# Kernel tuning notes

Hardware: AMD Instinct MI355X
Metric: run time of the kernel (lower is better)

Reference implementation:

```python
import jax, jax.numpy as jnp
import numpy as np

N, C, P, K = 100000, 64, 64, 16  # points, in_planes, planes, nsample
EPS = 1e-5

def _bn(y, g, b, m, v):
    # inference-mode batchnorm over channel (last) dim
    return (y - m) * (g * jax.lax.rsqrt(v + EPS)) + b

def setup_inputs() -> dict:
    key = jax.random.key(0)
    ks = jax.random.split(key, 12)
    p = jax.random.normal(ks[0], (N, 3), jnp.float32)
    x = jax.random.normal(ks[1], (N, C), jnp.float32)
    idx = jax.random.randint(ks[2], (N, K), 0, N, jnp.int32)
    s = 0.05
    w1 = jax.random.normal(ks[3], (C, P), jnp.float32) * s
    conv_w = jax.random.normal(ks[4], (P, P + 3), jnp.float32) * s  # Conv1d(P+3, P, 1) weight squeezed
    w3 = jax.random.normal(ks[5], (P, P), jnp.float32) * s
    def bn_params(k):
        k1, k2 = jax.random.split(k)
        return (jnp.ones((P,), jnp.float32),                      # gamma
                jnp.zeros((P,), jnp.float32),                     # beta
                jax.random.normal(k1, (P,), jnp.float32) * 0.01,  # running mean
                jnp.abs(jax.random.normal(k2, (P,), jnp.float32)) * 0.1 + 1.0)  # running var
    g1, b1, m1, v1 = bn_params(ks[6])
    g2, b2, m2, v2 = bn_params(ks[7])
    g3, b3, m3, v3 = bn_params(ks[8])
    return dict(p=p, x=x, idx=idx, w1=w1, g1=g1, b1=b1, m1=m1, v1=v1,
                conv_w=conv_w, g2=g2, b2=b2, m2=m2, v2=v2,
                w3=w3, g3=g3, b3=b3, m3=m3, v3=v3)

def reference(p, x, idx, w1, g1, b1, m1, v1, conv_w, g2, b2, m2, v2, w3, g3, b3, m3, v3):
    identity = x
    h = jax.nn.relu(_bn(x @ w1, g1, b1, m1, v1))                     # [N, P]
    # queryandgroup with use_xyz=True: concat(relative xyz, neighbor feats)
    rel = p[idx] - p[:, None, :]                                      # [N, K, 3]
    grouped = jnp.concatenate([rel, h[idx]], axis=-1)                 # [N, K, 3+P]
    e = jnp.einsum('nkc,oc->nko', grouped, conv_w)                    # conv1x1 -> [N, K, P]
    e = jax.nn.relu(_bn(e, g2, b2, m2, v2))
    f = jnp.max(e, axis=1)                                            # max over neighbors -> [N, P]
    out = jax.nn.relu(_bn(f @ w3, g3, b3, m3, v3) + identity)         # [N, P]
    return out
```

## Files before the change

### kernel.cpp

```cpp
#include <hip/hip_runtime.h>
#include <stdint.h>


#define EPS 1e-5f

typedef unsigned short u16;
typedef unsigned int u32;
typedef __attribute__((ext_vector_type(8))) short bf16x8;
typedef __attribute__((ext_vector_type(4))) float f32x4;

__device__ __forceinline__ float b2f(u16 u) { return __uint_as_float(((u32)u) << 16); }
__device__ __forceinline__ u16 f2b(float f) {
    u32 u = __float_as_uint(f);
    u32 r = u + 0x7fffu + ((u >> 16) & 1u);
    return (u16)(r >> 16);
}
__device__ __forceinline__ bool is_bf16(const void* g) { return ((const u32*)g)[0] == 0x3F803F80u; }
__device__ __forceinline__ float ldval(const void* p, size_t i, bool isbf) {
    return isbf ? b2f(((const u16*)p)[i]) : ((const float*)p)[i];
}
#define MFMA16(a, b, c) __builtin_amdgcn_mfma_f32_16x16x32_bf16(a, b, c, 0, 0, 0)

__device__ __forceinline__ bf16x8 asbf(uint4 u) {
    union { uint4 u; bf16x8 b; } c;
    c.u = u;
    return c.b;
}

__device__ __forceinline__ bf16x8 ldrow8(const void* base, size_t row, int coff, bool isbf) {
    if (isbf) {
        const u16* pp = (const u16*)base + row * 64 + coff;
        return asbf(*(const uint4*)pp);
    } else {
        const float* pp = (const float*)base + row * 64 + coff;
        float4 q0 = ((const float4*)pp)[0], q1 = ((const float4*)pp)[1];
        bf16x8 r;
        r[0] = (short)f2b(q0.x); r[1] = (short)f2b(q0.y);
        r[2] = (short)f2b(q0.z); r[3] = (short)f2b(q0.w);
        r[4] = (short)f2b(q1.x); r[5] = (short)f2b(q1.y);
        r[6] = (short)f2b(q1.z); r[7] = (short)f2b(q1.w);
        return r;
    }
}

__global__ void __launch_bounds__(256)
k_prep(const void* __restrict__ w1, const void* __restrict__ cw, const void* __restrict__ w3,
       const void* __restrict__ g1, const void* __restrict__ b1, const void* __restrict__ m1,
       const void* __restrict__ v1, const void* __restrict__ g2, const void* __restrict__ b2,
       const void* __restrict__ m2, const void* __restrict__ v2, const void* __restrict__ g3,
       const void* __restrict__ b3, const void* __restrict__ m3, const void* __restrict__ v3,
       uint4* __restrict__ w1f, uint4* __restrict__ cwf, uint4* __restrict__ w3f,
       float* __restrict__ bnst) {
    const bool isbf = is_bf16(g1);
    const int tid = blockIdx.x * blockDim.x + threadIdx.x;
    if (tid < 512) {
        int f = tid >> 6, lane = tid & 63;
        int ch = f >> 2, t = f & 3, quad = lane >> 4, c0 = lane & 15;
        union { uint4 u; bf16x8 b; } r;
#pragma unroll
        for (int j = 0; j < 8; ++j) {
            int c = ch * 32 + quad * 8 + j, o = t * 16 + c0;
            r.b[j] = (short)f2b(ldval(w1, (size_t)c * 64 + o, isbf));
        }
        w1f[f * 64 + lane] = r.u;
    } else if (tid < 1280) {
        int f = (tid - 512) >> 6, lane = tid & 63;
        int ch = f >> 2, t = f & 3, quad = lane >> 4, c0 = lane & 15;
        union { uint4 u; bf16x8 b; } r;
#pragma unroll
        for (int j = 0; j < 8; ++j) {
            int o = t * 16 + c0;
            short val;
            if (ch < 2) {
                int c = ch * 32 + quad * 8 + j;
                val = (short)f2b(ldval(cw, (size_t)o * 67 + 3 + c, isbf));
            } else {
                int pc = quad * 8 + j;
                val = (pc < 3) ? (short)f2b(ldval(cw, (size_t)o * 67 + pc, isbf)) : (short)0;
            }
            r.b[j] = val;
        }
        cwf[f * 64 + lane] = r.u;
    } else if (tid < 1792) {
        int f = (tid - 1280) >> 6, lane = tid & 63;
        int ch = f >> 2, t = f & 3, quad = lane >> 4, c0 = lane & 15;
        union { uint4 u; bf16x8 b; } r;
#pragma unroll
        for (int j = 0; j < 8; ++j) {
            int c = ch * 32 + quad * 8 + j, o = t * 16 + c0;
            r.b[j] = (short)f2b(ldval(w3, (size_t)c * 64 + o, isbf));
        }
        w3f[f * 64 + lane] = r.u;
    } else if (tid < 2176) {
        int id = tid - 1792;
        int bn = id >> 7, rem = id & 127, ch = rem & 63, which = rem >> 6;
        const void* g = (bn == 0) ? g1 : (bn == 1) ? g2 : g3;
        const void* b = (bn == 0) ? b1 : (bn == 1) ? b2 : b3;
        const void* m = (bn == 0) ? m1 : (bn == 1) ? m2 : m3;
        const void* v = (bn == 0) ? v1 : (bn == 1) ? v2 : v3;
        float gv = ldval(g, ch, isbf), bv = ldval(b, ch, isbf);
        float mv = ldval(m, ch, isbf), vv = ldval(v, ch, isbf);
        float s = gv * rsqrtf(vv + EPS);
        float t = bv - mv * s;
        bnst[bn * 128 + which * 64 + ch] = which ? t : s;
    }
}

__global__ void __launch_bounds__(256, 3)
k_hw_mfma(const void* __restrict__ x, const void* __restrict__ p, const void* __restrict__ g1,
          const uint4* __restrict__ w1f, const uint4* __restrict__ cwf,
          const float* __restrict__ bnst, u16* __restrict__ wbuf, u16* __restrict__ vbuf,
          int N) {
    const bool isbf = is_bf16(g1);
    const int lane = threadIdx.x & 63, quad = lane >> 4, col = lane & 15;
    const int wv = threadIdx.x >> 6;
    const int wave = blockIdx.x * (blockDim.x >> 6) + wv;
    const int nw = gridDim.x * (blockDim.x >> 6);
    __shared__ u16 hlds[4][16][72];
    f32x4 sv, tv;
#pragma unroll
    for (int t = 0; t < 4; ++t) {
        sv[t] = bnst[0 * 128 + 0 + t * 16 + col];
        tv[t] = bnst[0 * 128 + 64 + t * 16 + col];
    }
    bf16x8 W00 = asbf(w1f[0 * 64 + lane]), W01 = asbf(w1f[1 * 64 + lane]);
    bf16x8 W02 = asbf(w1f[2 * 64 + lane]), W03 = asbf(w1f[3 * 64 + lane]);
    bf16x8 W10 = asbf(w1f[4 * 64 + lane]), W11 = asbf(w1f[5 * 64 + lane]);
    bf16x8 W12 = asbf(w1f[6 * 64 + lane]), W13 = asbf(w1f[7 * 64 + lane]);
    bf16x8 B00 = asbf(cwf[0 * 64 + lane]), B01 = asbf(cwf[1 * 64 + lane]);
    bf16x8 B02 = asbf(cwf[2 * 64 + lane]), B03 = asbf(cwf[3 * 64 + lane]);
    bf16x8 B10 = asbf(cwf[4 * 64 + lane]), B11 = asbf(cwf[5 * 64 + lane]);
    bf16x8 B12 = asbf(cwf[6 * 64 + lane]), B13 = asbf(cwf[7 * 64 + lane]);
    bf16x8 B20 = asbf(cwf[8 * 64 + lane]), B21 = asbf(cwf[9 * 64 + lane]);
    bf16x8 B22 = asbf(cwf[10 * 64 + lane]), B23 = asbf(cwf[11 * 64 + lane]);
    const int nt = (N + 15) >> 4;
    for (int ti = wave; ti < nt; ti += nw) {
        const int n0 = ti * 16;
        int ra = n0 + col;
        if (ra > N - 1) ra = N - 1;
        bf16x8 A0 = ldrow8(x, (size_t)ra, quad * 8, isbf);
        bf16x8 A1 = ldrow8(x, (size_t)ra, 32 + quad * 8, isbf);
        f32x4 hc0 = {0.f, 0.f, 0.f, 0.f}, hc1 = hc0, hc2 = hc0, hc3 = hc0;
        hc0 = MFMA16(A0, W00, hc0); hc0 = MFMA16(A1, W10, hc0);
        hc1 = MFMA16(A0, W01, hc1); hc1 = MFMA16(A1, W11, hc1);
        hc2 = MFMA16(A0, W02, hc2); hc2 = MFMA16(A1, W12, hc2);
        hc3 = MFMA16(A0, W03, hc3); hc3 = MFMA16(A1, W13, hc3);
#define HST(acc, t)                                                            \
    {                                                                          \
        _Pragma("unroll") for (int r = 0; r < 4; ++r) {                        \
            hlds[wv][quad * 4 + r][(t)*16 + col] =                             \
                f2b(fmaxf(acc[r] * sv[t] + tv[t], 0.f));                       \
        }                                                                      \
    }
        HST(hc0, 0) HST(hc1, 1) HST(hc2, 2) HST(hc3, 3)
#undef HST
        bf16x8 hA0 = asbf(*(const uint4*)&hlds[wv][lane & 15][(lane >> 4) * 8]);
        bf16x8 hA1 = asbf(*(const uint4*)&hlds[wv][lane & 15][32 + (lane >> 4) * 8]);
        bf16x8 A2 = {0, 0, 0, 0, 0, 0, 0, 0};
        if (quad == 0) {
            A2[0] = (short)f2b(ldval(p, (size_t)ra * 3 + 0, isbf));
            A2[1] = (short)f2b(ldval(p, (size_t)ra * 3 + 1, isbf));
            A2[2] = (short)f2b(ldval(p, (size_t)ra * 3 + 2, isbf));
        }
        f32x4 z = {0.f, 0.f, 0.f, 0.f};
        f32x4 av0 = MFMA16(A2, B20, z), av1 = MFMA16(A2, B21, z);
        f32x4 av2 = MFMA16(A2, B22, z), av3 = MFMA16(A2, B23, z);
        f32x4 aw0 = MFMA16(hA1, B10, MFMA16(hA0, B00, av0));
        f32x4 aw1 = MFMA16(hA1, B11, MFMA16(hA0, B01, av1));
        f32x4 aw2 = MFMA16(hA1, B12, MFMA16(hA0, B02, av2));
        f32x4 aw3 = MFMA16(hA1, B13, MFMA16(hA0, B03, av3));
#define STW(accv, accw, t)                                                     \
    {                                                                          \
        _Pragma("unroll") for (int r = 0; r < 4; ++r) {                        \
            int row = n0 + quad * 4 + r;                                       \
            if (row < N) {                                                     \
                vbuf[(size_t)row * 64 + (t)*16 + col] = f2b(accv[r]);          \
                wbuf[(size_t)row * 64 + (t)*16 + col] = f2b(accw[r]);          \
            }                                                                  \
        }                                                                      \
    }
        STW(av0, aw0, 0) STW(av1, aw1, 1) STW(av2, aw2, 2) STW(av3, aw3, 3)
#undef STW
    }
}

__global__ void __launch_bounds__(256, 4)
k_h_mfma(const void* __restrict__ x, const void* __restrict__ p, const void* __restrict__ g1,
         const uint4* __restrict__ w1f, const float* __restrict__ bnst,
         float4* __restrict__ p4, u16* __restrict__ hbf, int N) {
    const bool isbf = is_bf16(g1);
    const int lane = threadIdx.x & 63, quad = lane >> 4, col = lane & 15;
    const int wave = blockIdx.x * (blockDim.x >> 6) + (threadIdx.x >> 6);
    const int nw = gridDim.x * (blockDim.x >> 6);
    bf16x8 B00 = asbf(w1f[0 * 64 + lane]), B01 = asbf(w1f[1 * 64 + lane]);
    bf16x8 B02 = asbf(w1f[2 * 64 + lane]), B03 = asbf(w1f[3 * 64 + lane]);
    bf16x8 B10 = asbf(w1f[4 * 64 + lane]), B11 = asbf(w1f[5 * 64 + lane]);
    bf16x8 B12 = asbf(w1f[6 * 64 + lane]), B13 = asbf(w1f[7 * 64 + lane]);
    f32x4 sv, tv;
#pragma unroll
    for (int t = 0; t < 4; ++t) {
        sv[t] = bnst[0 * 128 + 0 + t * 16 + col];
        tv[t] = bnst[0 * 128 + 64 + t * 16 + col];
    }
    const int nt = (N + 15) >> 4;
    for (int ti = wave; ti < nt; ti += nw) {
        const int n0 = ti * 16;
        int ra = n0 + col;
        if (ra > N - 1) ra = N - 1;
        bf16x8 A0 = ldrow8(x, (size_t)ra, quad * 8, isbf);
        bf16x8 A1 = ldrow8(x, (size_t)ra, 32 + quad * 8, isbf);
        if (p4 && quad == 0 && n0 + col < N) {
            int row = n0 + col;
            float4 pv;
            pv.x = ldval(p, (size_t)row * 3 + 0, isbf);
            pv.y = ldval(p, (size_t)row * 3 + 1, isbf);
            pv.z = ldval(p, (size_t)row * 3 + 2, isbf);
            pv.w = 0.f;
            p4[row] = pv;
        }
        f32x4 acc0 = {0.f, 0.f, 0.f, 0.f}, acc1 = acc0, acc2 = acc0, acc3 = acc0;
        acc0 = MFMA16(A0, B00, acc0); acc0 = MFMA16(A1, B10, acc0);
        acc1 = MFMA16(A0, B01, acc1); acc1 = MFMA16(A1, B11, acc1);
        acc2 = MFMA16(A0, B02, acc2); acc2 = MFMA16(A1, B12, acc2);
        acc3 = MFMA16(A0, B03, acc3); acc3 = MFMA16(A1, B13, acc3);
#define STT(acc, t)                                                            \
    {                                                                          \
        _Pragma("unroll") for (int r = 0; r < 4; ++r) {                        \
            int row = n0 + quad * 4 + r;                                       \
            if (row < N) {                                                     \
                float e = acc[r] * sv[t] + tv[t];                              \
                hbf[(size_t)row * 64 + (t)*16 + col] = f2b(fmaxf(e, 0.f));     \
            }                                                                  \
        }                                                                      \
    }
        STT(acc0, 0) STT(acc1, 1) STT(acc2, 2) STT(acc3, 3)
#undef STT
    }
}

__global__ void __launch_bounds__(256, 5)
k_gmax(const u16* __restrict__ wbuf, u16* __restrict__ vf, const int* __restrict__ idx,
       const float* __restrict__ bnst, int N) {
    const int lane = threadIdx.x & 63;
    const int wave = blockIdx.x * (blockDim.x >> 6) + (threadIdx.x >> 6);
    const int nw = gridDim.x * (blockDim.x >> 6);
    const float s2 = bnst[128 + lane];
    const float t2 = bnst[192 + lane];
    const int step = 4 * nw;
    int i = 4 * wave;
    if (i >= N) return;
    const size_t idxmax = (size_t)N * 16 - 1;
    size_t a0 = (size_t)i * 16 + lane;
    int jv = idx[a0 > idxmax ? idxmax : a0];
    for (; i < N; i += step) {
        size_t an = (size_t)(i + step) * 16 + lane;
        int jn = idx[an > idxmax ? idxmax : an];
        u32 wr0[16], wr1[16], wr2[16], wr3[16];
#pragma unroll
        for (int k = 0; k < 16; ++k) {
            int j0 = __builtin_amdgcn_readlane(jv, k);
            int j1 = __builtin_amdgcn_readlane(jv, 16 + k);
            int j2 = __builtin_amdgcn_readlane(jv, 32 + k);
            int j3 = __builtin_amdgcn_readlane(jv, 48 + k);
            wr0[k] = wbuf[(size_t)j0 * 64 + lane];
            wr1[k] = wbuf[(size_t)j1 * 64 + lane];
            wr2[k] = wbuf[(size_t)j2 * 64 + lane];
            wr3[k] = wbuf[(size_t)j3 * 64 + lane];
        }
        const int i1 = (i + 1 < N) ? i + 1 : i;
        const int i2 = (i + 2 < N) ? i + 2 : i;
        const int i3 = (i + 3 < N) ? i + 3 : i;
        u32 v0 = vf[(size_t)i * 64 + lane];
        u32 v1 = vf[(size_t)i1 * 64 + lane];
        u32 v2 = vf[(size_t)i2 * 64 + lane];
        u32 v3 = vf[(size_t)i3 * 64 + lane];
#define REDST(wr, vv, row, guard)                                              \
    {                                                                          \
        float mx = b2f((u16)wr[0]), mn = mx;                                   \
        _Pragma("unroll") for (int k = 1; k < 16; ++k) {                       \
            float fv_ = b2f((u16)wr[k]);                                       \
            mx = fmaxf(mx, fv_);                                               \
            mn = fminf(mn, fv_);                                               \
        }                                                                      \
        float e = fmaxf(s2 * mx, s2 * mn) + t2 - s2 * b2f((u16)vv);            \
        if (guard) vf[(size_t)(row)*64 + lane] = f2b(fmaxf(e, 0.f));           \
    }
        REDST(wr0, v0, i, true)
        REDST(wr1, v1, i + 1, (i + 1 < N))
        REDST(wr2, v2, i + 2, (i + 2 < N))
        REDST(wr3, v3, i + 3, (i + 3 < N))
#undef REDST
        jv = jn;
    }
}

template <bool FORCE_BF16>
__global__ void __launch_bounds__(256, 4)
k_conv_mfma(const u16* __restrict__ hbf, const float4* __restrict__ p4,
            const int* __restrict__ idx, const uint4* __restrict__ cwf,
            const float* __restrict__ bnst, const void* __restrict__ g2,
            void* __restrict__ fout, int N) {
    const bool isbf = is_bf16(g2);
    const int lane = threadIdx.x & 63, quad = lane >> 4, col = lane & 15;
    const int wave = blockIdx.x * (blockDim.x >> 6) + (threadIdx.x >> 6);
    const int nw = gridDim.x * (blockDim.x >> 6);
    bf16x8 B00 = asbf(cwf[0 * 64 + lane]), B01 = asbf(cwf[1 * 64 + lane]);
    bf16x8 B02 = asbf(cwf[2 * 64 + lane]), B03 = asbf(cwf[3 * 64 + lane]);
    bf16x8 B10 = asbf(cwf[4 * 64 + lane]), B11 = asbf(cwf[5 * 64 + lane]);
    bf16x8 B12 = asbf(cwf[6 * 64 + lane]), B13 = asbf(cwf[7 * 64 + lane]);
    bf16x8 B20 = asbf(cwf[8 * 64 + lane]), B21 = asbf(cwf[9 * 64 + lane]);
    bf16x8 B22 = asbf(cwf[10 * 64 + lane]), B23 = asbf(cwf[11 * 64 + lane]);
    f32x4 sv, tv;
#pragma unroll
    for (int t = 0; t < 4; ++t) {
        sv[t] = bnst[1 * 128 + 0 + t * 16 + col];
        tv[t] = bnst[1 * 128 + 64 + t * 16 + col];
    }
    int i = wave;
    if (i >= N) return;
    const int step = nw;
    int i1 = i + step;
    int i1c = (i1 < N) ? i1 : N - 1;
    int j0 = idx[(size_t)i * 16 + col];
    int j1 = idx[(size_t)i1c * 16 + col];
    const uint4* r0 = (const uint4*)(hbf + (size_t)j0 * 64);
    uint4 h0_c = r0[quad], h1_c = r0[4 + quad];
    float4 pj_c = p4[j0];
    float4 pn_c = p4[i];
    for (; i < N; i += step, i1 += step) {
        const int i2 = i1 + step;
        const int i2c = (i2 < N) ? i2 : N - 1;
        int j2 = idx[(size_t)i2c * 16 + col];
        const uint4* rn = (const uint4*)(hbf + (size_t)j1 * 64);
        uint4 h0_n = rn[quad], h1_n = rn[4 + quad];
        const int i1cc = (i1 < N) ? i1 : N - 1;
        float4 pj_n = p4[j1];
        float4 pn_n = p4[i1cc];
        bf16x8 A2 = {0, 0, 0, 0, 0, 0, 0, 0};
        if (quad == 0) {
            A2[0] = (short)f2b(pj_c.x - pn_c.x);
            A2[1] = (short)f2b(pj_c.y - pn_c.y);
            A2[2] = (short)f2b(pj_c.z - pn_c.z);
        }
        f32x4 z = {0.f, 0.f, 0.f, 0.f};
        f32x4 acc0 = z, acc1 = z, acc2 = z, acc3 = z;
        bf16x8 a0 = asbf(h0_c), a1 = asbf(h1_c);
        acc0 = MFMA16(a0, B00, acc0);
        acc1 = MFMA16(a0, B01, acc1);
        acc2 = MFMA16(a0, B02, acc2);
        acc3 = MFMA16(a0, B03, acc3);
        acc0 = MFMA16(a1, B10, acc0);
        acc1 = MFMA16(a1, B11, acc1);
        acc2 = MFMA16(a1, B12, acc2);
        acc3 = MFMA16(a1, B13, acc3);
        acc0 = MFMA16(A2, B20, acc0);
        acc1 = MFMA16(A2, B21, acc1);
        acc2 = MFMA16(A2, B22, acc2);
        acc3 = MFMA16(A2, B23, acc3);
#define RED(acc, t, dst)                                                       \
    {                                                                          \
        float mx = fmaxf(fmaxf(acc[0], acc[1]), fmaxf(acc[2], acc[3]));        \
        float mn = fminf(fminf(acc[0], acc[1]), fminf(acc[2], acc[3]));        \
        mx = fmaxf(mx, __shfl_xor(mx, 16));                                    \
        mn = fminf(mn, __shfl_xor(mn, 16));                                    \
        mx = fmaxf(mx, __shfl_xor(mx, 32));                                    \
        mn = fminf(mn, __shfl_xor(mn, 32));                                    \
        float e = fmaxf(sv[t] * mx + tv[t], sv[t] * mn + tv[t]);               \
        dst = fmaxf(e, 0.f);                                                   \
    }
        float f0, f1, f2, f3;
        RED(acc0, 0, f0) RED(acc1, 1, f1) RED(acc2, 2, f2) RED(acc3, 3, f3)
#undef RED
        float fv = (lane < 16) ? f0 : (lane < 32) ? f1 : (lane < 48) ? f2 : f3;
        if (FORCE_BF16 || isbf)
            ((u16*)fout)[(size_t)i * 64 + lane] = f2b(fv);
        else
            ((float*)fout)[(size_t)i * 64 + lane] = fv;
        j0 = j1; j1 = j2;
        h0_c = h0_n; h1_c = h1_n;
        pj_c = pj_n; pn_c = pn_n;
    }
}

template <bool FIN_BF16_ALWAYS>
__global__ void __launch_bounds__(256, 4)
k_out_mfma(const void* __restrict__ fin, const void* __restrict__ x,
           const uint4* __restrict__ w3f, const float* __restrict__ bnst,
           const void* __restrict__ g3, void* __restrict__ out, int N) {
    const bool isbf = is_bf16(g3);
    const bool finbf = FIN_BF16_ALWAYS ? true : isbf;
    const int lane = threadIdx.x & 63, quad = lane >> 4, col = lane & 15;
    const int wave = blockIdx.x * (blockDim.x >> 6) + (threadIdx.x >> 6);
    const int nw = gridDim.x * (blockDim.x >> 6);
    bf16x8 B00 = asbf(w3f[0 * 64 + lane]), B01 = asbf(w3f[1 * 64 + lane]);
    bf16x8 B02 = asbf(w3f[2 * 64 + lane]), B03 = asbf(w3f[3 * 64 + lane]);
    bf16x8 B10 = asbf(w3f[4 * 64 + lane]), B11 = asbf(w3f[5 * 64 + lane]);
    bf16x8 B12 = asbf(w3f[6 * 64 + lane]), B13 = asbf(w3f[7 * 64 + lane]);
    f32x4 sv, tv;
#pragma unroll
    for (int t = 0; t < 4; ++t) {
        sv[t] = bnst[2 * 128 + 0 + t * 16 + col];
        tv[t] = bnst[2 * 128 + 64 + t * 16 + col];
    }
    const int nt = (N + 15) >> 4;
    for (int ti = wave; ti < nt; ti += nw) {
        const int n0 = ti * 16;
        int ra = n0 + col;
        if (ra > N - 1) ra = N - 1;
        bf16x8 A0 = ldrow8(fin, (size_t)ra, quad * 8, finbf);
        bf16x8 A1 = ldrow8(fin, (size_t)ra, 32 + quad * 8, finbf);
        f32x4 acc0 = {0.f, 0.f, 0.f, 0.f}, acc1 = acc0, acc2 = acc0, acc3 = acc0;
        acc0 = MFMA16(A0, B00, acc0); acc0 = MFMA16(A1, B10, acc0);
        acc1 = MFMA16(A0, B01, acc1); acc1 = MFMA16(A1, B11, acc1);
        acc2 = MFMA16(A0, B02, acc2); acc2 = MFMA16(A1, B12, acc2);
        acc3 = MFMA16(A0, B03, acc3); acc3 = MFMA16(A1, B13, acc3);
#define STT(acc, t)                                                            \
    {                                                                          \
        _Pragma("unroll") for (int r = 0; r < 4; ++r) {                        \
            int row = n0 + quad * 4 + r;                                       \
            if (row < N) {                                                     \
                int o_ = (t)*16 + col;                                         \
                float e = acc[r] * sv[t] + tv[t] +                             \
                          ldval(x, (size_t)row * 64 + o_, isbf);               \
                e = fmaxf(e, 0.f);                                             \
                if (isbf)                                                      \
                    ((u16*)out)[(size_t)row * 64 + o_] = f2b(e);               \
                else                                                           \
                    ((float*)out)[(size_t)row * 64 + o_] = e;                  \
            }                                                                  \
        }                                                                      \
    }
        STT(acc0, 0) STT(acc1, 1) STT(acc2, 2) STT(acc3, 3)
#undef STT
    }
}

__device__ __forceinline__ void load_col64(const void* w, int lane, bool isbf, float* col) {
#pragma unroll
    for (int c = 0; c < 64; ++c) col[c] = ldval(w, (size_t)c * 64 + lane, isbf);
}
__device__ __forceinline__ float dot64(const void* x, size_t off, bool isbf, const float* col) {
    float a0 = 0.f;
#pragma unroll
    for (int c = 0; c < 64; ++c) a0 += ldval(x, off + c, isbf) * col[c];
    return a0;
}
__device__ __forceinline__ void bn_st(const void* g, const void* b, const void* m,
                                      const void* v, int o, bool isbf, float& s, float& t) {
    float gv = ldval(g, o, isbf), bv = ldval(b, o, isbf);
    float mv = ldval(m, o, isbf), vv = ldval(v, o, isbf);
    s = gv * rsqrtf(vv + EPS);
    t = bv - mv * s;
}
__global__ void __launch_bounds__(256) k_mono(const void* __restrict__ p, const void* __restrict__ x,
                                              const int* __restrict__ idx, const void* __restrict__ w1,
                                              const void* __restrict__ g1, const void* __restrict__ b1,
                                              const void* __restrict__ m1, const void* __restrict__ v1,
                                              const void* __restrict__ cw, const void* __restrict__ g2,
                                              const void* __restrict__ b2, const void* __restrict__ m2,
                                              const void* __restrict__ v2, const void* __restrict__ w3,
                                              const void* __restrict__ g3, const void* __restrict__ b3,
                                              const void* __restrict__ m3, const void* __restrict__ v3,
                                              void* __restrict__ out, int N) {
    const bool isbf = is_bf16(g1);
    const int lane = threadIdx.x & 63;
    const int wave = blockIdx.x * (blockDim.x >> 6) + (threadIdx.x >> 6);
    const int nw = gridDim.x * (blockDim.x >> 6);
    float w1col[64];
    load_col64(w1, lane, isbf, w1col);
    float w3col[64];
    load_col64(w3, lane, isbf, w3col);
    float s1, t1, s2, t2, s3, t3;
    bn_st(g1, b1, m1, v1, lane, isbf, s1, t1);
    bn_st(g2, b2, m2, v2, lane, isbf, s2, t2);
    bn_st(g3, b3, m3, v3, lane, isbf, s3, t3);
    for (int n = wave; n < N; n += nw) {
        const int4* ir = (const int4*)(idx + (size_t)n * 16);
        float pnx = ldval(p, (size_t)n * 3 + 0, isbf);
        float pny = ldval(p, (size_t)n * 3 + 1, isbf);
        float pnz = ldval(p, (size_t)n * 3 + 2, isbf);
        float fmx = 0.f;
        for (int kk = 0; kk < 4; ++kk) {
            const int4 iv = ir[kk];
#pragma unroll
            for (int t = 0; t < 4; ++t) {
                const int j = (t == 0) ? iv.x : (t == 1) ? iv.y : (t == 2) ? iv.z : iv.w;
                float hr = dot64(x, (size_t)j * 64, isbf, w1col);
                float hv = fmaxf(hr * s1 + t1, 0.f);
                float a0 = (ldval(p, (size_t)j * 3 + 0, isbf) - pnx) * ldval(cw, (size_t)lane * 67 + 0, isbf) +
                           (ldval(p, (size_t)j * 3 + 1, isbf) - pny) * ldval(cw, (size_t)lane * 67 + 1, isbf) +
                           (ldval(p, (size_t)j * 3 + 2, isbf) - pnz) * ldval(cw, (size_t)lane * 67 + 2, isbf);
#pragma unroll
                for (int c = 0; c < 64; ++c)
                    a0 += __shfl(hv, c) * ldval(cw, (size_t)lane * 67 + 3 + c, isbf);
                fmx = fmaxf(fmx, a0 * s2 + t2);
            }
        }
        float a = 0.f;
#pragma unroll
        for (int c = 0; c < 64; ++c) a += __shfl(fmx, c) * w3col[c];
        float r = a * s3 + t3 + ldval(x, (size_t)n * 64 + lane, isbf);
        r = fmaxf(r, 0.f);
        if (isbf)
            ((u16*)out)[(size_t)n * 64 + lane] = f2b(r);
        else
            ((float*)out)[(size_t)n * 64 + lane] = r;
    }
}

extern "C" void kernel_launch(void* const* d_in, const int* in_sizes, int n_in,
                              void* d_out, int out_size, void* d_ws, size_t ws_size,
                              hipStream_t stream) {
    const void* p = d_in[0];
    const void* x = d_in[1];
    const int* idx = (const int*)d_in[2];
    const void* w1 = d_in[3];
    const void* g1 = d_in[4];
    const void* b1 = d_in[5];
    const void* m1 = d_in[6];
    const void* v1 = d_in[7];
    const void* cw = d_in[8];
    const void* g2 = d_in[9];
    const void* b2 = d_in[10];
    const void* m2 = d_in[11];
    const void* v2 = d_in[12];
    const void* w3 = d_in[13];
    const void* g3 = d_in[14];
    const void* b3 = d_in[15];
    const void* m3 = d_in[16];
    const void* v3 = d_in[17];
    const int N = in_sizes[0] / 3;

    const int blk = 256;
    const int nt = (N + 15) >> 4;
    const int gh = (nt + 3) >> 2;
    const int gg = 1280;

    const size_t hb = (size_t)N * 64 * sizeof(u16);
    const size_t p4b = (size_t)N * sizeof(float4);
    const size_t packb = 8192 + 12288 + 8192 + 1536;
    const size_t need_big = 256 + 2 * hb + packb;
    const size_t need_h = 256 + hb + p4b + packb;

    if (ws_size >= need_big) {
        char* base = (char*)d_ws + 256;
        u16* b1buf = (u16*)base;
        u16* b2buf = (u16*)(base + hb);
        char* rest = base + 2 * hb;
        uint4* w1f = (uint4*)rest;
        uint4* cwf = (uint4*)(rest + 8192);
        uint4* w3f = (uint4*)(rest + 8192 + 12288);
        float* bnst = (float*)(rest + 8192 + 12288 + 8192);
        k_prep<<<9, blk, 0, stream>>>(w1, cw, w3, g1, b1, m1, v1, g2, b2, m2, v2,
                                      g3, b3, m3, v3, w1f, cwf, w3f, bnst);
        k_hw_mfma<<<gh, blk, 0, stream>>>(x, p, g1, w1f, cwf, bnst, b1buf, b2buf, N);
        k_gmax<<<gg, blk, 0, stream>>>(b1buf, b2buf, idx, bnst, N);
        k_out_mfma<true><<<gh, blk, 0, stream>>>((const void*)b2buf, x, w3f, bnst, g3,
                                                 d_out, N);
    } else if (ws_size >= need_h) {
        char* base = (char*)d_ws + 256;
        u16* h = (u16*)base;
        char* rest = base + hb;
        float4* p4 = (float4*)rest;
        uint4* w1f = (uint4*)(rest + p4b);
        uint4* cwf = (uint4*)(rest + p4b + 8192);
        uint4* w3f = (uint4*)(rest + p4b + 8192 + 12288);
        float* bnst = (float*)(rest + p4b + 8192 + 12288 + 8192);
        k_prep<<<9, blk, 0, stream>>>(w1, cw, w3, g1, b1, m1, v1, g2, b2, m2, v2,
                                      g3, b3, m3, v3, w1f, cwf, w3f, bnst);
        k_h_mfma<<<gh, blk, 0, stream>>>(x, p, g1, w1f, bnst, p4, h, N);
        k_conv_mfma<false><<<2048, blk, 0, stream>>>(h, p4, idx, cwf, bnst, g2, d_out, N);
        k_out_mfma<false><<<gh, blk, 0, stream>>>((const void*)d_out, x, w3f, bnst, g3,
                                                  d_out, N);
    } else {
        k_mono<<<2048, blk, 0, stream>>>(p, x, idx, w1, g1, b1, m1, v1, cw, g2, b2, m2, v2,
                                         w3, g3, b3, m3, v3, d_out, N);
    }
}
```

Baseline: 170.2 us.

## Fuse neighbor gather-max with output projection GEMM into one kernel

Replaces the separate gather-max kernel and the output MFMA kernel with one kernel, k_gout. It stages each wave's reduced feature rows in LDS, then every four iterations runs the w3 projection with BN3, the residual add and ReLU in-register before writing the output. This removes the global write and re-read of the intermediate feature buffer and one kernel launch. In exchange it raises per-wave register and LDS use (launch bounds drop to 3 waves per SIMD, grid reduced to 768 blocks) and writes output rows in scattered groups of four.

```diff
diff --git a/kernel.cpp b/kernel.cpp
--- a/kernel.cpp
+++ b/kernel.cpp
@@ -238,20 +238,66 @@
     }
 }
 
-__global__ void __launch_bounds__(256, 5)
-k_gmax(const u16* __restrict__ wbuf, u16* __restrict__ vf, const int* __restrict__ idx,
-       const float* __restrict__ bnst, int N) {
-    const int lane = threadIdx.x & 63;
-    const int wave = blockIdx.x * (blockDim.x >> 6) + (threadIdx.x >> 6);
-    const int nw = gridDim.x * (blockDim.x >> 6);
+__global__ void __launch_bounds__(256, 3)
+k_gout(const u16* __restrict__ wbuf, const u16* __restrict__ vf, const int* __restrict__ idx,
+       const uint4* __restrict__ w3f, const float* __restrict__ bnst,
+       const void* __restrict__ x, const void* __restrict__ g3,
+       void* __restrict__ out, int N) {
+    const bool isbf = is_bf16(g3);
+    const int lane = threadIdx.x & 63, quad = lane >> 4, col = lane & 15;
+    const int wv = threadIdx.x >> 6;
+    const int wave = blockIdx.x * 4 + wv;
+    const int nw = gridDim.x * 4;
+    __shared__ u16 flds[4][16][72];
     const float s2 = bnst[128 + lane];
     const float t2 = bnst[192 + lane];
+    f32x4 sv3, tv3;
+#pragma unroll
+    for (int t = 0; t < 4; ++t) {
+        sv3[t] = bnst[256 + t * 16 + col];
+        tv3[t] = bnst[320 + t * 16 + col];
+    }
+    bf16x8 W00 = asbf(w3f[0 * 64 + lane]), W01 = asbf(w3f[1 * 64 + lane]);
+    bf16x8 W02 = asbf(w3f[2 * 64 + lane]), W03 = asbf(w3f[3 * 64 + lane]);
+    bf16x8 W10 = asbf(w3f[4 * 64 + lane]), W11 = asbf(w3f[5 * 64 + lane]);
+    bf16x8 W12 = asbf(w3f[6 * 64 + lane]), W13 = asbf(w3f[7 * 64 + lane]);
     const int step = 4 * nw;
     int i = 4 * wave;
     if (i >= N) return;
     const size_t idxmax = (size_t)N * 16 - 1;
     size_t a0 = (size_t)i * 16 + lane;
     int jv = idx[a0 > idxmax ? idxmax : a0];
+    int sub = 0;
+    int ridb = -1;
+#define OUTFLUSH()                                                             \
+    {                                                                          \
+        bf16x8 fA0 = asbf(*(const uint4*)&flds[wv][lane & 15][(lane >> 4) * 8]); \
+        bf16x8 fA1 = asbf(*(const uint4*)&flds[wv][lane & 15][32 + (lane >> 4) * 8]); \
+        f32x4 zz = {0.f, 0.f, 0.f, 0.f};                                       \
+        f32x4 ac0 = zz, ac1 = zz, ac2 = zz, ac3 = zz;                          \
+        ac0 = MFMA16(fA0, W00, ac0); ac0 = MFMA16(fA1, W10, ac0);              \
+        ac1 = MFMA16(fA0, W01, ac1); ac1 = MFMA16(fA1, W11, ac1);              \
+        ac2 = MFMA16(fA0, W02, ac2); ac2 = MFMA16(fA1, W12, ac2);              \
+        ac3 = MFMA16(fA0, W03, ac3); ac3 = MFMA16(fA1, W13, ac3);              \
+        if (ridb >= 0) {                                                       \
+            _Pragma("unroll") for (int t = 0; t < 4; ++t) {                    \
+                f32x4 ac = (t == 0) ? ac0 : (t == 1) ? ac1 : (t == 2) ? ac2 : ac3; \
+                _Pragma("unroll") for (int r = 0; r < 4; ++r) {                \
+                    int row = ridb + r;                                        \
+                    if (row < N) {                                             \
+                        int o_ = t * 16 + col;                                 \
+                        float e = ac[r] * sv3[t] + tv3[t] +                    \
+                                  ldval(x, (size_t)row * 64 + o_, isbf);       \
+                        e = fmaxf(e, 0.f);                                     \
+                        if (isbf)                                              \
+                            ((u16*)out)[(size_t)row * 64 + o_] = f2b(e);       \
+                        else                                                   \
+                            ((float*)out)[(size_t)row * 64 + o_] = e;          \
+                    }                                                          \
+                }                                                              \
+            }                                                                  \
+        }                                                                      \
+    }
     for (; i < N; i += step) {
         size_t an = (size_t)(i + step) * 16 + lane;
         int jn = idx[an > idxmax ? idxmax : an];
@@ -274,7 +320,7 @@
         u32 v1 = vf[(size_t)i1 * 64 + lane];
         u32 v2 = vf[(size_t)i2 * 64 + lane];
         u32 v3 = vf[(size_t)i3 * 64 + lane];
-#define REDST(wr, vv, row, guard)                                              \
+#define REDST(wr, vv, r_)                                                      \
     {                                                                          \
         float mx = b2f((u16)wr[0]), mn = mx;                                   \
         _Pragma("unroll") for (int k = 1; k < 16; ++k) {                       \
@@ -283,15 +329,24 @@
             mn = fminf(mn, fv_);                                               \
         }                                                                      \
         float e = fmaxf(s2 * mx, s2 * mn) + t2 - s2 * b2f((u16)vv);            \
-        if (guard) vf[(size_t)(row)*64 + lane] = f2b(fmaxf(e, 0.f));           \
-    }
-        REDST(wr0, v0, i, true)
-        REDST(wr1, v1, i + 1, (i + 1 < N))
-        REDST(wr2, v2, i + 2, (i + 2 < N))
-        REDST(wr3, v3, i + 3, (i + 3 < N))
+        flds[wv][sub * 4 + (r_)][lane] = f2b(fmaxf(e, 0.f));                   \
+    }
+        REDST(wr0, v0, 0)
+        REDST(wr1, v1, 1)
+        REDST(wr2, v2, 2)
+        REDST(wr3, v3, 3)
 #undef REDST
+        if (quad == sub) ridb = i;
+        ++sub;
+        if (sub == 4) {
+            OUTFLUSH()
+            sub = 0;
+            ridb = -1;
+        }
         jv = jn;
     }
+    if (sub != 0) { OUTFLUSH() }
+#undef OUTFLUSH
 }
 
 template <bool FORCE_BF16>
@@ -534,7 +589,7 @@
     const int blk = 256;
     const int nt = (N + 15) >> 4;
     const int gh = (nt + 3) >> 2;
-    const int gg = 1280;
+    const int gg = 768;
 
     const size_t hb = (size_t)N * 64 * sizeof(u16);
     const size_t p4b = (size_t)N * sizeof(float4);
@@ -554,9 +609,7 @@
         k_prep<<<9, blk, 0, stream>>>(w1, cw, w3, g1, b1, m1, v1, g2, b2, m2, v2,
                                       g3, b3, m3, v3, w1f, cwf, w3f, bnst);
         k_hw_mfma<<<gh, blk, 0, stream>>>(x, p, g1, w1f, cwf, bnst, b1buf, b2buf, N);
-        k_gmax<<<gg, blk, 0, stream>>>(b1buf, b2buf, idx, bnst, N);
-        k_out_mfma<true><<<gh, blk, 0, stream>>>((const void*)b2buf, x, w3f, bnst, g3,
-                                                 d_out, N);
+        k_gout<<<gg, blk, 0, stream>>>(b1buf, b2buf, idx, w3f, bnst, x, g3, d_out, N);
     } else if (ws_size >= need_h) {
         char* base = (char*)d_ws + 256;
         u16* h = (u16*)base;
```

Result: no change. 170.4 us (+0.1%).
